# Performance work log

Measured on AMD Instinct MI355X. Metric: run time of the kernel, lower is better.

Reference implementation:

```python
import jax, jax.numpy as jnp
import numpy as np

LN_EPS = 1e-5

def setup_inputs() -> dict:
    key = jax.random.key(0)
    ks = jax.random.split(key, 5)
    B, S, Dv, Dl, V = 4, 576, 1024, 4096, 32000
    return {
        "vision_feats": jax.random.normal(ks[0], (B, S, Dv), dtype=jnp.float32),
        "W1_w": jax.random.normal(ks[1], (Dl, Dv), dtype=jnp.float32) * (Dv ** -0.5),
        "W1_b": jax.random.normal(ks[2], (Dl,), dtype=jnp.float32) * 0.02,
        "W2_w": jax.random.normal(ks[3], (V, Dl), dtype=jnp.float32) * (Dl ** -0.5),
        "llm_token_embed": jax.random.normal(ks[4], (V, Dl), dtype=jnp.float32) * 0.02,
    }

def reference(vision_feats, W1_w, W1_b, W2_w, llm_token_embed):
    # W1: (B,S,Dv) @ (Dv,Dl) + b -> (B,S,Dl)
    x = jnp.einsum('bsd,ed->bse', vision_feats, W1_w) + W1_b
    # layer_norm over last dim, no affine params
    mu = jnp.mean(x, axis=-1, keepdims=True)
    var = jnp.mean(jnp.square(x - mu), axis=-1, keepdims=True)
    xn = (x - mu) * jax.lax.rsqrt(var + LN_EPS)
    # W2 (no bias): (B,S,Dl) -> (B,S,V) vocab logits
    logits = jnp.einsum('bse,ve->bsv', xn, W2_w)
    P = jax.nn.softmax(logits, axis=-1)
    # softmax-weighted mixture of LLM token embeddings: (B,S,V) @ (V,Dl)
    F_align = jnp.einsum('bsv,ve->bse', P, llm_token_embed)
    return F_align
```

## Files before the change

kernel.cpp:

```cpp
#include <hip/hip_runtime.h>
#include <hip/hip_bf16.h>
#include <stdint.h>

typedef __bf16 bf16_t;
typedef __attribute__((ext_vector_type(8))) __bf16 bf16x8;
typedef __attribute__((ext_vector_type(4))) __bf16 bf16x4;
typedef __attribute__((ext_vector_type(4))) float f32x4;
typedef __attribute__((ext_vector_type(8))) unsigned short u16x8;

#define M_TOK 2304
#define DV    1024
#define DLAT  4096
#define VOCAB 32000

__device__ __forceinline__ float bf2f(unsigned short u) {
  union { unsigned int i; float f; } v; v.i = ((unsigned int)u) << 16; return v.f;
}
__device__ __forceinline__ bf16_t f2bf(float f) { return (bf16_t)f; }

#define GLOAD16(gp, lp) \
  __builtin_amdgcn_global_load_lds( \
      (const __attribute__((address_space(1))) unsigned int*)(const void*)(gp), \
      (__attribute__((address_space(3))) unsigned int*)(void*)(lp), 16, 0, 0)

constexpr int GBM = 128, GBN = 128, GBK = 32;

template<int EPI>
__global__ void __launch_bounds__(256, 3)
gemm_bb(const bf16_t* __restrict__ Ap, const bf16_t* __restrict__ Bp,
        void* __restrict__ Cp, const float* __restrict__ bias,
        int K, int ldc, int Mt)
{
  __shared__ __align__(16) bf16_t Al[3][GBM * GBK];
  __shared__ __align__(16) bf16_t Bl[3][GBN * GBK];

  const int nwg = gridDim.x;
  const int orig = blockIdx.x;
  const int q = nwg >> 3, r = nwg & 7;
  const int xcd = orig & 7, idx = orig >> 3;
  const int wg = (xcd < r ? xcd * (q + 1) : r * (q + 1) + (xcd - r) * q) + idx;
  const int mt = wg % Mt, nt = wg / Mt;
  const int m0 = mt * GBM, n0 = nt * GBN;

  const int t    = threadIdx.x;
  const int lane = t & 63, wv = t >> 6;
  const int wm = wv >> 1, wn = wv & 1;
  const int lr = lane & 15, kc = lane >> 4;

  f32x4 acc[4][4];
#pragma unroll
  for (int i = 0; i < 4; ++i)
#pragma unroll
    for (int j = 0; j < 4; ++j)
#pragma unroll
      for (int x = 0; x < 4; ++x) acc[i][j][x] = 0.0f;

  const int rql = lane >> 2;
  const int cbs = (((lane & 3) ^ ((lane >> 3) & 3)) * 16);
  const size_t rstride = (size_t)K * 2;

  const int sw8 = (kc ^ ((lr >> 1) & 3)) * 8;

  const int NT = K / GBK;

  auto STAGE = [&](int kt, int nb) {
    const size_t kb = (size_t)kt * GBK * 2;
    const char* ga = (const char*)Ap + (size_t)(m0 + wv * 32 + rql) * rstride + kb + cbs;
    char* la = (char*)&Al[nb][0] + wv * 2048;
    GLOAD16(ga, la);
    GLOAD16(ga + 16 * rstride, la + 1024);
    const char* gb = (const char*)Bp + (size_t)(n0 + wv * 32 + rql) * rstride + kb + cbs;
    char* lb = (char*)&Bl[nb][0] + wv * 2048;
    GLOAD16(gb, lb);
    GLOAD16(gb + 16 * rstride, lb + 1024);
  };

  auto COMPUTE = [&](int nb) {
    bf16x8 af[4], bfv[4];
#pragma unroll
    for (int f = 0; f < 4; ++f)
      af[f] = *(const bf16x8*)(&Al[nb][(wm * 64 + f * 16 + lr) * GBK + sw8]);
#pragma unroll
    for (int f = 0; f < 4; ++f)
      bfv[f] = *(const bf16x8*)(&Bl[nb][(wn * 64 + f * 16 + lr) * GBK + sw8]);
    __builtin_amdgcn_s_setprio(1);
#pragma unroll
    for (int i = 0; i < 4; ++i)
#pragma unroll
      for (int j = 0; j < 4; ++j)
        acc[i][j] = __builtin_amdgcn_mfma_f32_16x16x32_bf16(af[i], bfv[j], acc[i][j], 0, 0, 0);
    __builtin_amdgcn_s_setprio(0);
  };

  auto BARX = [&]() {
    asm volatile("s_waitcnt lgkmcnt(0)" ::: "memory");
    __builtin_amdgcn_s_barrier();
  };

  STAGE(0, 0);
  STAGE(1, 1);
  asm volatile("s_waitcnt vmcnt(4)" ::: "memory");
  __builtin_amdgcn_s_barrier();

  int bc = 0, bn = 1, bs = 2;
  for (int kt = 0; kt < NT - 2; ++kt) {
    STAGE(kt + 2, bs);
    COMPUTE(bc);
    asm volatile("s_waitcnt vmcnt(4)" ::: "memory");
    BARX();
    const int tmp = bc; bc = bn; bn = bs; bs = tmp;
  }
  COMPUTE(bc);
  asm volatile("s_waitcnt vmcnt(0)" ::: "memory");
  BARX();
  COMPUTE(bn);

#pragma unroll
  for (int j = 0; j < 4; ++j) {
    const int col = n0 + wn * 64 + j * 16 + lr;
    float bv = 0.0f;
    if (EPI == 0) bv = bias[col];
#pragma unroll
    for (int i = 0; i < 4; ++i) {
      const int row = m0 + wm * 64 + i * 16 + kc * 4;
      f32x4 a4 = acc[i][j];
      if (EPI == 1) {
        bf16_t* C = (bf16_t*)Cp;
#pragma unroll
        for (int x = 0; x < 4; ++x) C[(size_t)(row + x) * ldc + col] = f2bf(a4[x]);
      } else {
        float* C = (float*)Cp;
#pragma unroll
        for (int x = 0; x < 4; ++x) C[(size_t)(row + x) * ldc + col] = a4[x] + bv;
      }
    }
  }
}

constexpr int BM = 128, BN = 128, BK = 32;
constexpr int SA = 40;

__device__ __forceinline__ void bar_lds() {
  asm volatile("s_waitcnt lgkmcnt(0)" ::: "memory");
  __builtin_amdgcn_s_barrier();
}

template<int AMODE, int BMODE, int EPI>
__global__ void __launch_bounds__(256, 2)
gemm_k(const void* __restrict__ Ap, const float* __restrict__ Bp,
       void* __restrict__ Cp, const float* __restrict__ bias,
       int K, int lda, int ldb, int ldc, int Mt)
{
  __shared__ __align__(16) bf16_t Al[2][BM * SA];
  __shared__ __align__(16) bf16_t Bl[2][BN * SA];

  const int nwg = gridDim.x;
  const int orig = blockIdx.x;
  const int q = nwg >> 3, r = nwg & 7;
  const int xcd = orig & 7, idx = orig >> 3;
  const int wg = (xcd < r ? xcd * (q + 1) : r * (q + 1) + (xcd - r) * q) + idx;
  const int mt = wg % Mt, nt = wg / Mt;
  const int m0 = mt * BM, n0 = nt * BN;

  const int t    = threadIdx.x;
  const int lane = t & 63, wv = t >> 6;
  const int wm = wv >> 1, wn = wv & 1;
  const int lr = lane & 15, kc = lane >> 4;

  f32x4 acc[4][4];
#pragma unroll
  for (int i = 0; i < 4; ++i)
#pragma unroll
    for (int j = 0; j < 4; ++j)
#pragma unroll
      for (int x = 0; x < 4; ++x) acc[i][j][x] = 0.0f;

  const int sr = t >> 1, sh = t & 1;
  const int tv = t & 7, te = t >> 3;

  bf16x8 s1_ab0, s1_ab1;          bf16x8 s2_ab0, s2_ab1;
  f32x4  s1_af0, s1_af1, s1_af2, s1_af3;
  f32x4  s2_af0, s2_af1, s2_af2, s2_af3;
  f32x4  s1_b0, s1_b1, s1_b2, s1_b3;
  f32x4  s2_b0, s2_b1, s2_b2, s2_b3;

  const int NT = K / BK;

  auto LOADS1 = [&](int kt) {
    const int k0 = kt * BK;
    if (AMODE == 0) {
      const bf16_t* asrc = (const bf16_t*)Ap + (size_t)(m0 + sr) * lda + k0 + sh * 16;
      s1_ab0 = *(const bf16x8*)(asrc);
      s1_ab1 = *(const bf16x8*)(asrc + 8);
    } else {
      const float* asrc = (const float*)Ap + (size_t)(m0 + sr) * lda + k0 + sh * 16;
      s1_af0 = *(const f32x4*)(asrc);     s1_af1 = *(const f32x4*)(asrc + 4);
      s1_af2 = *(const f32x4*)(asrc + 8); s1_af3 = *(const f32x4*)(asrc + 12);
    }
    if (BMODE == 0) {
      const float* bsrc = Bp + (size_t)(n0 + sr) * ldb + k0 + sh * 16;
      s1_b0 = *(const f32x4*)(bsrc);     s1_b1 = *(const f32x4*)(bsrc + 4);
      s1_b2 = *(const f32x4*)(bsrc + 8); s1_b3 = *(const f32x4*)(bsrc + 12);
    } else {
      const float* bsrc = Bp + (size_t)(k0 + tv * 4) * ldb + n0 + te * 4;
      s1_b0 = *(const f32x4*)(bsrc);
      s1_b1 = *(const f32x4*)(bsrc + (size_t)ldb);
      s1_b2 = *(const f32x4*)(bsrc + (size_t)2 * ldb);
      s1_b3 = *(const f32x4*)(bsrc + (size_t)3 * ldb);
    }
  };
  auto LOADS2 = [&](int kt) {
    const int k0 = kt * BK;
    if (AMODE == 0) {
      const bf16_t* asrc = (const bf16_t*)Ap + (size_t)(m0 + sr) * lda + k0 + sh * 16;
      s2_ab0 = *(const bf16x8*)(asrc);
      s2_ab1 = *(const bf16x8*)(asrc + 8);
    } else {
      const float* asrc = (const float*)Ap + (size_t)(m0 + sr) * lda + k0 + sh * 16;
      s2_af0 = *(const f32x4*)(asrc);     s2_af1 = *(const f32x4*)(asrc + 4);
      s2_af2 = *(const f32x4*)(asrc + 8); s2_af3 = *(const f32x4*)(asrc + 12);
    }
    if (BMODE == 0) {
      const float* bsrc = Bp + (size_t)(n0 + sr) * ldb + k0 + sh * 16;
      s2_b0 = *(const f32x4*)(bsrc);     s2_b1 = *(const f32x4*)(bsrc + 4);
      s2_b2 = *(const f32x4*)(bsrc + 8); s2_b3 = *(const f32x4*)(bsrc + 12);
    } else {
      const float* bsrc = Bp + (size_t)(k0 + tv * 4) * ldb + n0 + te * 4;
      s2_b0 = *(const f32x4*)(bsrc);
      s2_b1 = *(const f32x4*)(bsrc + (size_t)ldb);
      s2_b2 = *(const f32x4*)(bsrc + (size_t)2 * ldb);
      s2_b3 = *(const f32x4*)(bsrc + (size_t)3 * ldb);
    }
  };

  auto STORE1 = [&](int nb) {
    {
      bf16x8 w0, w1;
      if (AMODE == 0) { w0 = s1_ab0; w1 = s1_ab1; }
      else {
#pragma unroll
        for (int c = 0; c < 4; ++c) {
          w0[c] = f2bf(s1_af0[c]); w0[c + 4] = f2bf(s1_af1[c]);
          w1[c] = f2bf(s1_af2[c]); w1[c + 4] = f2bf(s1_af3[c]);
        }
      }
      bf16_t* dst = &Al[nb][sr * SA + sh * 16];
      *(bf16x8*)(dst) = w0; *(bf16x8*)(dst + 8) = w1;
    }
    if (BMODE == 0) {
      bf16x8 w0, w1;
#pragma unroll
      for (int c = 0; c < 4; ++c) {
        w0[c] = f2bf(s1_b0[c]); w0[c + 4] = f2bf(s1_b1[c]);
        w1[c] = f2bf(s1_b2[c]); w1[c + 4] = f2bf(s1_b3[c]);
      }
      bf16_t* dst = &Bl[nb][sr * SA + sh * 16];
      *(bf16x8*)(dst) = w0; *(bf16x8*)(dst + 8) = w1;
    } else {
#pragma unroll
      for (int i = 0; i < 4; ++i) {
        bf16x4 w4;
        w4[0] = f2bf(s1_b0[i]); w4[1] = f2bf(s1_b1[i]);
        w4[2] = f2bf(s1_b2[i]); w4[3] = f2bf(s1_b3[i]);
        *(bf16x4*)(&Bl[nb][(te * 4 + i) * SA + tv * 4]) = w4;
      }
    }
  };
  auto STORE2 = [&](int nb) {
    {
      bf16x8 w0, w1;
      if (AMODE == 0) { w0 = s2_ab0; w1 = s2_ab1; }
      else {
#pragma unroll
        for (int c = 0; c < 4; ++c) {
          w0[c] = f2bf(s2_af0[c]); w0[c + 4] = f2bf(s2_af1[c]);
          w1[c] = f2bf(s2_af2[c]); w1[c + 4] = f2bf(s2_af3[c]);
        }
      }
      bf16_t* dst = &Al[nb][sr * SA + sh * 16];
      *(bf16x8*)(dst) = w0; *(bf16x8*)(dst + 8) = w1;
    }
    if (BMODE == 0) {
      bf16x8 w0, w1;
#pragma unroll
      for (int c = 0; c < 4; ++c) {
        w0[c] = f2bf(s2_b0[c]); w0[c + 4] = f2bf(s2_b1[c]);
        w1[c] = f2bf(s2_b2[c]); w1[c + 4] = f2bf(s2_b3[c]);
      }
      bf16_t* dst = &Bl[nb][sr * SA + sh * 16];
      *(bf16x8*)(dst) = w0; *(bf16x8*)(dst + 8) = w1;
    } else {
#pragma unroll
      for (int i = 0; i < 4; ++i) {
        bf16x4 w4;
        w4[0] = f2bf(s2_b0[i]); w4[1] = f2bf(s2_b1[i]);
        w4[2] = f2bf(s2_b2[i]); w4[3] = f2bf(s2_b3[i]);
        *(bf16x4*)(&Bl[nb][(te * 4 + i) * SA + tv * 4]) = w4;
      }
    }
  };

  auto COMPUTE = [&](int nb) {
    bf16x8 af[4], bfv[4];
#pragma unroll
    for (int f = 0; f < 4; ++f)
      af[f] = *(const bf16x8*)(&Al[nb][(wm * 64 + f * 16 + lr) * SA + kc * 8]);
#pragma unroll
    for (int f = 0; f < 4; ++f)
      bfv[f] = *(const bf16x8*)(&Bl[nb][(wn * 64 + f * 16 + lr) * SA + kc * 8]);
    __builtin_amdgcn_s_setprio(1);
#pragma unroll
    for (int i = 0; i < 4; ++i)
#pragma unroll
      for (int j = 0; j < 4; ++j)
        acc[i][j] = __builtin_amdgcn_mfma_f32_16x16x32_bf16(af[i], bfv[j], acc[i][j], 0, 0, 0);
    __builtin_amdgcn_s_setprio(0);
  };

  LOADS1(0);
  LOADS2(1);
  STORE1(0);
  bar_lds();

  const int NIT = NT / 2 - 1;
  for (int it = 0; it < NIT; ++it) {
    LOADS1(2 * it + 2);
    COMPUTE(0);
    STORE2(1);
    bar_lds();
    LOADS2(2 * it + 3);
    COMPUTE(1);
    STORE1(0);
    bar_lds();
  }
  COMPUTE(0);
  STORE2(1);
  bar_lds();
  COMPUTE(1);

#pragma unroll
  for (int j = 0; j < 4; ++j) {
    const int col = n0 + wn * 64 + j * 16 + lr;
    float bv = 0.0f;
    if (EPI == 0) bv = bias[col];
#pragma unroll
    for (int i = 0; i < 4; ++i) {
      const int row = m0 + wm * 64 + i * 16 + kc * 4;
      f32x4 a4 = acc[i][j];
      if (EPI == 0) {
        float* C = (float*)Cp;
#pragma unroll
        for (int x = 0; x < 4; ++x) C[(size_t)(row + x) * ldc + col] = a4[x] + bv;
      } else if (EPI == 1) {
        bf16_t* C = (bf16_t*)Cp;
#pragma unroll
        for (int x = 0; x < 4; ++x) C[(size_t)(row + x) * ldc + col] = f2bf(a4[x]);
      } else {
        float* C = (float*)Cp;
#pragma unroll
        for (int x = 0; x < 4; ++x) C[(size_t)(row + x) * ldc + col] = a4[x];
      }
    }
  }
}

__global__ void __launch_bounds__(256)
cvt_bf16_k(const float* __restrict__ in, bf16_t* __restrict__ out, long n8)
{
  const long stride = (long)gridDim.x * 256;
  for (long i = (long)blockIdx.x * 256 + threadIdx.x; i < n8; i += stride) {
    f32x4 a = *(const f32x4*)(in + i * 8);
    f32x4 b = *(const f32x4*)(in + i * 8 + 4);
    bf16x8 o;
#pragma unroll
    for (int j = 0; j < 4; ++j) { o[j] = f2bf(a[j]); o[j + 4] = f2bf(b[j]); }
    *(bf16x8*)(out + i * 8) = o;
  }
}

__global__ void __launch_bounds__(256)
embT_k(const float* __restrict__ E, bf16_t* __restrict__ ET)
{
  __shared__ bf16_t tl[64][72];
  const int vb = blockIdx.x % (VOCAB / 64);
  const int eb = blockIdx.x / (VOCAB / 64);
  const int v0 = vb * 64, e0 = eb * 64;
  const int t = threadIdx.x;

  const int rr = t >> 4, c4 = (t & 15) * 4;
#pragma unroll
  for (int p = 0; p < 4; ++p) {
    const float* src = E + (size_t)(v0 + rr + p * 16) * DLAT + e0 + c4;
    f32x4 a = *(const f32x4*)src;
#pragma unroll
    for (int j = 0; j < 4; ++j) tl[c4 + j][rr + p * 16] = f2bf(a[j]);
  }
  __syncthreads();

  const int el = t >> 3, v8 = (t & 7) * 8;
#pragma unroll
  for (int p = 0; p < 2; ++p) {
    bf16x8 o = *(const bf16x8*)(&tl[el + p * 32][v8]);
    *(bf16x8*)(ET + (size_t)(e0 + el + p * 32) * VOCAB + v0 + v8) = o;
  }
}

__global__ void __launch_bounds__(256)
ln_k(const float* __restrict__ x, bf16_t* __restrict__ xn)
{
  __shared__ float sm[4];
  const int row = blockIdx.x, t = threadIdx.x;
  const float* xr = x + (size_t)row * DLAT;
  f32x4 v[4];
#pragma unroll
  for (int i = 0; i < 4; ++i) v[i] = *(const f32x4*)(xr + (t + i * 256) * 4);

  float s = 0.0f;
#pragma unroll
  for (int i = 0; i < 4; ++i)
#pragma unroll
    for (int j = 0; j < 4; ++j) s += v[i][j];
#pragma unroll
  for (int o = 32; o > 0; o >>= 1) s += __shfl_xor(s, o, 64);
  if ((t & 63) == 0) sm[t >> 6] = s;
  __syncthreads();
  const float mean = (sm[0] + sm[1] + sm[2] + sm[3]) * (1.0f / DLAT);
  __syncthreads();

  float qv = 0.0f;
#pragma unroll
  for (int i = 0; i < 4; ++i)
#pragma unroll
    for (int j = 0; j < 4; ++j) { float d = v[i][j] - mean; qv += d * d; }
#pragma unroll
  for (int o = 32; o > 0; o >>= 1) qv += __shfl_xor(qv, o, 64);
  if ((t & 63) == 0) sm[t >> 6] = qv;
  __syncthreads();
  const float varr = (sm[0] + sm[1] + sm[2] + sm[3]) * (1.0f / DLAT);
  const float rs = rsqrtf(varr + 1e-5f);

  bf16_t* outr = xn + (size_t)row * DLAT;
#pragma unroll
  for (int i = 0; i < 4; ++i) {
    bf16x4 o;
#pragma unroll
    for (int j = 0; j < 4; ++j) o[j] = f2bf((v[i][j] - mean) * rs);
    *(bf16x4*)(outr + (t + i * 256) * 4) = o;
  }
}

__global__ void __launch_bounds__(256)
softmax_k(bf16_t* __restrict__ L)
{
  __shared__ __align__(16) bf16_t rs_[VOCAB];
  __shared__ float sm[4];
  const int row = blockIdx.x, t = threadIdx.x;
  bf16_t* lrow = L + (size_t)row * VOCAB;
  const int NF = VOCAB / 8;

  float m = -3.0e38f;
  for (int f = t; f < NF; f += 256) {
    u16x8 u = *(const u16x8*)(&lrow[f * 8]);
    *(u16x8*)(&rs_[f * 8]) = u;
#pragma unroll
    for (int j = 0; j < 8; ++j) m = fmaxf(m, bf2f(u[j]));
  }
#pragma unroll
  for (int o = 32; o > 0; o >>= 1) m = fmaxf(m, __shfl_xor(m, o, 64));
  if ((t & 63) == 0) sm[t >> 6] = m;
  __syncthreads();
  m = fmaxf(fmaxf(sm[0], sm[1]), fmaxf(sm[2], sm[3]));
  __syncthreads();

  float s = 0.0f;
  for (int f = t; f < NF; f += 256) {
    u16x8 u = *(const u16x8*)(&rs_[f * 8]);
#pragma unroll
    for (int j = 0; j < 8; ++j) s += __expf(bf2f(u[j]) - m);
  }
#pragma unroll
  for (int o = 32; o > 0; o >>= 1) s += __shfl_xor(s, o, 64);
  if ((t & 63) == 0) sm[t >> 6] = s;
  __syncthreads();
  const float inv = 1.0f / (sm[0] + sm[1] + sm[2] + sm[3]);

  for (int f = t; f < NF; f += 256) {
    u16x8 u = *(const u16x8*)(&rs_[f * 8]);
    bf16x8 o;
#pragma unroll
    for (int j = 0; j < 8; ++j) o[j] = f2bf(__expf(bf2f(u[j]) - m) * inv);
    *(bf16x8*)(&lrow[f * 8]) = o;
  }
}

extern "C" void kernel_launch(void* const* d_in, const int* in_sizes, int n_in,
                              void* d_out, int out_size, void* d_ws, size_t ws_size,
                              hipStream_t stream)
{
  (void)in_sizes; (void)n_in; (void)out_size;
  const float* vision = (const float*)d_in[0];
  const float* W1w    = (const float*)d_in[1];
  const float* W1b    = (const float*)d_in[2];
  const float* W2w    = (const float*)d_in[3];
  const float* Emb    = (const float*)d_in[4];
  float* out = (float*)d_out;

  char* ws = (char*)d_ws;
  bf16_t* xn     = (bf16_t*)ws;
  bf16_t* logits = (bf16_t*)(ws + 18874368);
  float*  xbuf   = (float*)(ws + 166330368);
  bf16_t* wslot  = (bf16_t*)(ws + 204079104);
  bf16_t* xnv    = (bf16_t*)(ws + 466223104);
  bf16_t* w1b    = (bf16_t*)(ws + 470941696);
  const size_t NEED = 479330304ull;

  const int Mt = M_TOK / GBM;

  if (ws_size >= NEED) {
    cvt_bf16_k<<<dim3(512), dim3(256), 0, stream>>>(vision, xnv, (long)M_TOK * DV / 8);
    cvt_bf16_k<<<dim3(512), dim3(256), 0, stream>>>(W1w, w1b, (long)DLAT * DV / 8);
    gemm_bb<0><<<dim3(Mt * (DLAT / GBN)), dim3(256), 0, stream>>>(
        xnv, w1b, xbuf, W1b, DV, DLAT, Mt);
    ln_k<<<dim3(M_TOK), dim3(256), 0, stream>>>(xbuf, xn);
    cvt_bf16_k<<<dim3(2048), dim3(256), 0, stream>>>(W2w, wslot, (long)VOCAB * DLAT / 8);
    gemm_bb<1><<<dim3(Mt * (VOCAB / GBN)), dim3(256), 0, stream>>>(
        xn, wslot, logits, nullptr, DLAT, VOCAB, Mt);
    embT_k<<<dim3((VOCAB / 64) * (DLAT / 64)), dim3(256), 0, stream>>>(Emb, wslot);
    softmax_k<<<dim3(M_TOK), dim3(256), 0, stream>>>(logits);
    gemm_bb<2><<<dim3(Mt * (DLAT / GBN)), dim3(256), 0, stream>>>(
        logits, wslot, out, nullptr, VOCAB, DLAT, Mt);
  } else {
    gemm_k<1, 0, 0><<<dim3((M_TOK / BM) * (DLAT / BN)), dim3(256), 0, stream>>>(
        vision, W1w, xbuf, W1b, DV, DV, DV, DLAT, M_TOK / BM);
    ln_k<<<dim3(M_TOK), dim3(256), 0, stream>>>(xbuf, xn);
    gemm_k<0, 0, 1><<<dim3((M_TOK / BM) * (VOCAB / BN)), dim3(256), 0, stream>>>(
        xn, W2w, logits, nullptr, DLAT, DLAT, DLAT, VOCAB, M_TOK / BM);
    softmax_k<<<dim3(M_TOK), dim3(256), 0, stream>>>(logits);
    gemm_k<0, 1, 2><<<dim3((M_TOK / BM) * (DLAT / BN)), dim3(256), 0, stream>>>(
        logits, Emb, out, nullptr, VOCAB, VOCAB, DLAT, DLAT, M_TOK / BM);
  }
}
```

Before: 1.955 ms.

## Use 256-row 512-thread GEMM tiles for vocab GEMMs with split-K final GEMM

Adds a gemm256 kernel with 256xBN tiles, 8 waves, a triple-buffered direct-to-LDS pipeline and staged loads interleaved with MFMA phases. It replaces the 128x128 kernel for the logits GEMM and for the softmax-times-embedding GEMM. The latter is split into two K halves whose partials are summed by a small add kernel. It also removes the fp32 fallback path that ran when the workspace was too small. The intent is more data reuse per tile and better CU fill on the final GEMM, at the cost of extra partial-sum traffic and an extra launch.

Result: slower. 2.300 ms (+17.7%).

```diff
diff --git a/kernel.cpp b/kernel.cpp
--- a/kernel.cpp
+++ b/kernel.cpp
@@ -22,6 +22,148 @@
   __builtin_amdgcn_global_load_lds( \
       (const __attribute__((address_space(1))) unsigned int*)(const void*)(gp), \
       (__attribute__((address_space(3))) unsigned int*)(void*)(lp), 16, 0, 0)
+
+template<int BN_, int WM_, int WN_, int EPI, int MINW>
+__global__ void __launch_bounds__(512, MINW)
+gemm256(const bf16_t* __restrict__ Ap, const bf16_t* __restrict__ Bp,
+        void* __restrict__ Cp0, void* __restrict__ Cp1,
+        int Ksplit, int ld, int ldc, int Mt, int Nt)
+{
+  constexpr int WMR = 256 / WM_;
+  constexpr int NFM = WMR / 16;
+  constexpr int NFN = (BN_ / WN_) / 16;
+  constexpr int PM  = NFM / 4;
+  constexpr int BLOADS = BN_ / 128;
+  constexpr int L = 2 + BLOADS;
+
+  __shared__ __align__(16) bf16_t Al[3][256 * 32];
+  __shared__ __align__(16) bf16_t Bl[3][BN_ * 32];
+
+  const int nwg = gridDim.x;
+  const int orig = blockIdx.x;
+  const int q = nwg >> 3, r = nwg & 7;
+  const int xcd = orig & 7, idx = orig >> 3;
+  const int wg = (xcd < r ? xcd * (q + 1) : r * (q + 1) + (xcd - r) * q) + idx;
+  const int mt = wg % Mt;
+  const int nt = (wg / Mt) % Nt;
+  const int sp = wg / (Mt * Nt);
+  const int m0 = mt * 256, n0 = nt * BN_;
+  const int kb0 = sp * Ksplit;
+
+  const int t    = threadIdx.x;
+  const int lane = t & 63, wv = t >> 6;
+  const int wm = wv / WN_, wn = wv % WN_;
+  const int lr = lane & 15, kc = lane >> 4;
+
+  const int rql = lane >> 2;
+  const int cbs = (((lane & 3) ^ ((lane >> 3) & 3)) * 16);
+  const int sw8 = (kc ^ ((lr >> 1) & 3)) * 8;
+  const size_t rstride = (size_t)ld * 2;
+
+  f32x4 acc[NFM][NFN];
+#pragma unroll
+  for (int i = 0; i < NFM; ++i)
+#pragma unroll
+    for (int j = 0; j < NFN; ++j)
+#pragma unroll
+      for (int x = 0; x < 4; ++x) acc[i][j][x] = 0.0f;
+
+  const int NT = Ksplit / 32;
+
+  auto SG = [&](int kt, int nb, int which) {
+    const size_t kb = (size_t)(kb0 + kt * 32) * 2;
+    if (which < 2) {
+      const char* g = (const char*)Ap + (size_t)(m0 + wv * 32 + rql) * rstride
+                      + (size_t)which * 16 * rstride + kb + cbs;
+      char* l = (char*)&Al[nb][0] + wv * 2048 + which * 1024;
+      GLOAD16(g, l);
+    } else if (BLOADS == 2) {
+      const int w2 = which - 2;
+      const char* g = (const char*)Bp + (size_t)(n0 + wv * 32 + rql) * rstride
+                      + (size_t)w2 * 16 * rstride + kb + cbs;
+      char* l = (char*)&Bl[nb][0] + wv * 2048 + w2 * 1024;
+      GLOAD16(g, l);
+    } else {
+      const char* g = (const char*)Bp + (size_t)(n0 + wv * 16 + rql) * rstride + kb + cbs;
+      char* l = (char*)&Bl[nb][0] + wv * 1024;
+      GLOAD16(g, l);
+    }
+  };
+
+  auto TILE = [&](int bc, int bs, int kt, int stg, int wait) {
+    bf16x8 bfv[NFN];
+#pragma unroll
+    for (int p = 0; p < 4; ++p) {
+      bf16x8 af[PM];
+      if (p == 0) {
+#pragma unroll
+        for (int g = 0; g < NFN; ++g)
+          bfv[g] = *(const bf16x8*)(&Bl[bc][(wn * 64 + g * 16 + lr) * 32 + sw8]);
+      }
+#pragma unroll
+      for (int s = 0; s < PM; ++s)
+        af[s] = *(const bf16x8*)(&Al[bc][(wm * WMR + (p * PM + s) * 16 + lr) * 32 + sw8]);
+      if (stg) {
+        if (p < 2) SG(kt + 2, bs, p);
+        else if (p - 2 < BLOADS) SG(kt + 2, bs, p);
+      }
+      if (p == 3) {
+        if (wait == 1) {
+          if constexpr (L == 4) asm volatile("s_waitcnt vmcnt(4)" ::: "memory");
+          else                  asm volatile("s_waitcnt vmcnt(3)" ::: "memory");
+        } else if (wait == 2) {
+          asm volatile("s_waitcnt vmcnt(0)" ::: "memory");
+        }
+      }
+      __builtin_amdgcn_s_barrier();
+      __builtin_amdgcn_s_setprio(1);
+#pragma unroll
+      for (int s = 0; s < PM; ++s)
+#pragma unroll
+        for (int g = 0; g < NFN; ++g)
+          acc[p * PM + s][g] =
+            __builtin_amdgcn_mfma_f32_16x16x32_bf16(af[s], bfv[g], acc[p * PM + s][g], 0, 0, 0);
+      __builtin_amdgcn_s_setprio(0);
+    }
+  };
+
+#pragma unroll
+  for (int w = 0; w < L; ++w) SG(0, 0, w);
+#pragma unroll
+  for (int w = 0; w < L; ++w) SG(1, 1, w);
+  if constexpr (L == 4) asm volatile("s_waitcnt vmcnt(4)" ::: "memory");
+  else                  asm volatile("s_waitcnt vmcnt(3)" ::: "memory");
+  __builtin_amdgcn_s_barrier();
+
+  int c0 = 0, c1 = 1, c2 = 2;
+  int kt = 0;
+  for (; kt < NT - 2; ++kt) {
+    TILE(c0, c2, kt, 1, 1);
+    const int tmp = c0; c0 = c1; c1 = c2; c2 = tmp;
+  }
+  TILE(c0, c2, kt, 0, 2);
+  { const int tmp = c0; c0 = c1; c1 = c2; c2 = tmp; }
+  TILE(c0, c2, kt + 1, 0, 0);
+
+  float* Cf = (EPI == 2) ? (sp == 0 ? (float*)Cp0 : (float*)Cp1) : (float*)Cp0;
+#pragma unroll
+  for (int j = 0; j < NFN; ++j) {
+    const int col = n0 + wn * 64 + j * 16 + lr;
+#pragma unroll
+    for (int i = 0; i < NFM; ++i) {
+      const int row = m0 + wm * WMR + i * 16 + kc * 4;
+      f32x4 a4 = acc[i][j];
+      if (EPI == 1) {
+        bf16_t* C = (bf16_t*)Cp0;
+#pragma unroll
+        for (int x = 0; x < 4; ++x) C[(size_t)(row + x) * ldc + col] = f2bf(a4[x]);
+      } else {
+#pragma unroll
+        for (int x = 0; x < 4; ++x) Cf[(size_t)(row + x) * ldc + col] = a4[x];
+      }
+    }
+  }
+}
 
 constexpr int GBM = 128, GBN = 128, GBK = 32;
 
@@ -57,9 +199,8 @@
 
   const int rql = lane >> 2;
   const int cbs = (((lane & 3) ^ ((lane >> 3) & 3)) * 16);
+  const int sw8 = (kc ^ ((lr >> 1) & 3)) * 8;
   const size_t rstride = (size_t)K * 2;
-
-  const int sw8 = (kc ^ ((lr >> 1) & 3)) * 8;
 
   const int NT = K / GBK;
 
@@ -137,230 +278,16 @@
   }
 }
 
-constexpr int BM = 128, BN = 128, BK = 32;
-constexpr int SA = 40;
-
-__device__ __forceinline__ void bar_lds() {
-  asm volatile("s_waitcnt lgkmcnt(0)" ::: "memory");
-  __builtin_amdgcn_s_barrier();
-}
-
-template<int AMODE, int BMODE, int EPI>
-__global__ void __launch_bounds__(256, 2)
-gemm_k(const void* __restrict__ Ap, const float* __restrict__ Bp,
-       void* __restrict__ Cp, const float* __restrict__ bias,
-       int K, int lda, int ldb, int ldc, int Mt)
-{
-  __shared__ __align__(16) bf16_t Al[2][BM * SA];
-  __shared__ __align__(16) bf16_t Bl[2][BN * SA];
-
-  const int nwg = gridDim.x;
-  const int orig = blockIdx.x;
-  const int q = nwg >> 3, r = nwg & 7;
-  const int xcd = orig & 7, idx = orig >> 3;
-  const int wg = (xcd < r ? xcd * (q + 1) : r * (q + 1) + (xcd - r) * q) + idx;
-  const int mt = wg % Mt, nt = wg / Mt;
-  const int m0 = mt * BM, n0 = nt * BN;
-
-  const int t    = threadIdx.x;
-  const int lane = t & 63, wv = t >> 6;
-  const int wm = wv >> 1, wn = wv & 1;
-  const int lr = lane & 15, kc = lane >> 4;
-
-  f32x4 acc[4][4];
-#pragma unroll
-  for (int i = 0; i < 4; ++i)
-#pragma unroll
-    for (int j = 0; j < 4; ++j)
-#pragma unroll
-      for (int x = 0; x < 4; ++x) acc[i][j][x] = 0.0f;
-
-  const int sr = t >> 1, sh = t & 1;
-  const int tv = t & 7, te = t >> 3;
-
-  bf16x8 s1_ab0, s1_ab1;          bf16x8 s2_ab0, s2_ab1;
-  f32x4  s1_af0, s1_af1, s1_af2, s1_af3;
-  f32x4  s2_af0, s2_af1, s2_af2, s2_af3;
-  f32x4  s1_b0, s1_b1, s1_b2, s1_b3;
-  f32x4  s2_b0, s2_b1, s2_b2, s2_b3;
-
-  const int NT = K / BK;
-
-  auto LOADS1 = [&](int kt) {
-    const int k0 = kt * BK;
-    if (AMODE == 0) {
-      const bf16_t* asrc = (const bf16_t*)Ap + (size_t)(m0 + sr) * lda + k0 + sh * 16;
-      s1_ab0 = *(const bf16x8*)(asrc);
-      s1_ab1 = *(const bf16x8*)(asrc + 8);
-    } else {
-      const float* asrc = (const float*)Ap + (size_t)(m0 + sr) * lda + k0 + sh * 16;
-      s1_af0 = *(const f32x4*)(asrc);     s1_af1 = *(const f32x4*)(asrc + 4);
-      s1_af2 = *(const f32x4*)(asrc + 8); s1_af3 = *(const f32x4*)(asrc + 12);
-    }
-    if (BMODE == 0) {
-      const float* bsrc = Bp + (size_t)(n0 + sr) * ldb + k0 + sh * 16;
-      s1_b0 = *(const f32x4*)(bsrc);     s1_b1 = *(const f32x4*)(bsrc + 4);
-      s1_b2 = *(const f32x4*)(bsrc + 8); s1_b3 = *(const f32x4*)(bsrc + 12);
-    } else {
-      const float* bsrc = Bp + (size_t)(k0 + tv * 4) * ldb + n0 + te * 4;
-      s1_b0 = *(const f32x4*)(bsrc);
-      s1_b1 = *(const f32x4*)(bsrc + (size_t)ldb);
-      s1_b2 = *(const f32x4*)(bsrc + (size_t)2 * ldb);
-      s1_b3 = *(const f32x4*)(bsrc + (size_t)3 * ldb);
-    }
-  };
-  auto LOADS2 = [&](int kt) {
-    const int k0 = kt * BK;
-    if (AMODE == 0) {
-      const bf16_t* asrc = (const bf16_t*)Ap + (size_t)(m0 + sr) * lda + k0 + sh * 16;
-      s2_ab0 = *(const bf16x8*)(asrc);
-      s2_ab1 = *(const bf16x8*)(asrc + 8);
-    } else {
-      const float* asrc = (const float*)Ap + (size_t)(m0 + sr) * lda + k0 + sh * 16;
-      s2_af0 = *(const f32x4*)(asrc);     s2_af1 = *(const f32x4*)(asrc + 4);
-      s2_af2 = *(const f32x4*)(asrc + 8); s2_af3 = *(const f32x4*)(asrc + 12);
-    }
-    if (BMODE == 0) {
-      const float* bsrc = Bp + (size_t)(n0 + sr) * ldb + k0 + sh * 16;
-      s2_b0 = *(const f32x4*)(bsrc);     s2_b1 = *(const f32x4*)(bsrc + 4);
-      s2_b2 = *(const f32x4*)(bsrc + 8); s2_b3 = *(const f32x4*)(bsrc + 12);
-    } else {
-      const float* bsrc = Bp + (size_t)(k0 + tv * 4) * ldb + n0 + te * 4;
-      s2_b0 = *(const f32x4*)(bsrc);
-      s2_b1 = *(const f32x4*)(bsrc + (size_t)ldb);
-      s2_b2 = *(const f32x4*)(bsrc + (size_t)2 * ldb);
-      s2_b3 = *(const f32x4*)(bsrc + (size_t)3 * ldb);
-    }
-  };
-
-  auto STORE1 = [&](int nb) {
-    {
-      bf16x8 w0, w1;
-      if (AMODE == 0) { w0 = s1_ab0; w1 = s1_ab1; }
-      else {
-#pragma unroll
-        for (int c = 0; c < 4; ++c) {
-          w0[c] = f2bf(s1_af0[c]); w0[c + 4] = f2bf(s1_af1[c]);
-          w1[c] = f2bf(s1_af2[c]); w1[c + 4] = f2bf(s1_af3[c]);
-        }
-      }
-      bf16_t* dst = &Al[nb][sr * SA + sh * 16];
-      *(bf16x8*)(dst) = w0; *(bf16x8*)(dst + 8) = w1;
-    }
-    if (BMODE == 0) {
-      bf16x8 w0, w1;
-#pragma unroll
-      for (int c = 0; c < 4; ++c) {
-        w0[c] = f2bf(s1_b0[c]); w0[c + 4] = f2bf(s1_b1[c]);
-        w1[c] = f2bf(s1_b2[c]); w1[c + 4] = f2bf(s1_b3[c]);
-      }
-      bf16_t* dst = &Bl[nb][sr * SA + sh * 16];
-      *(bf16x8*)(dst) = w0; *(bf16x8*)(dst + 8) = w1;
-    } else {
-#pragma unroll
-      for (int i = 0; i < 4; ++i) {
-        bf16x4 w4;
-        w4[0] = f2bf(s1_b0[i]); w4[1] = f2bf(s1_b1[i]);
-        w4[2] = f2bf(s1_b2[i]); w4[3] = f2bf(s1_b3[i]);
-        *(bf16x4*)(&Bl[nb][(te * 4 + i) * SA + tv * 4]) = w4;
-      }
-    }
-  };
-  auto STORE2 = [&](int nb) {
-    {
-      bf16x8 w0, w1;
-      if (AMODE == 0) { w0 = s2_ab0; w1 = s2_ab1; }
-      else {
-#pragma unroll
-        for (int c = 0; c < 4; ++c) {
-          w0[c] = f2bf(s2_af0[c]); w0[c + 4] = f2bf(s2_af1[c]);
-          w1[c] = f2bf(s2_af2[c]); w1[c + 4] = f2bf(s2_af3[c]);
-        }
-      }
-      bf16_t* dst = &Al[nb][sr * SA + sh * 16];
-      *(bf16x8*)(dst) = w0; *(bf16x8*)(dst + 8) = w1;
-    }
-    if (BMODE == 0) {
-      bf16x8 w0, w1;
-#pragma unroll
-      for (int c = 0; c < 4; ++c) {
-        w0[c] = f2bf(s2_b0[c]); w0[c + 4] = f2bf(s2_b1[c]);
-        w1[c] = f2bf(s2_b2[c]); w1[c + 4] = f2bf(s2_b3[c]);
-      }
-      bf16_t* dst = &Bl[nb][sr * SA + sh * 16];
-      *(bf16x8*)(dst) = w0; *(bf16x8*)(dst + 8) = w1;
-    } else {
-#pragma unroll
-      for (int i = 0; i < 4; ++i) {
-        bf16x4 w4;
-        w4[0] = f2bf(s2_b0[i]); w4[1] = f2bf(s2_b1[i]);
-        w4[2] = f2bf(s2_b2[i]); w4[3] = f2bf(s2_b3[i]);
-        *(bf16x4*)(&Bl[nb][(te * 4 + i) * SA + tv * 4]) = w4;
-      }
-    }
-  };
-
-  auto COMPUTE = [&](int nb) {
-    bf16x8 af[4], bfv[4];
-#pragma unroll
-    for (int f = 0; f < 4; ++f)
-      af[f] = *(const bf16x8*)(&Al[nb][(wm * 64 + f * 16 + lr) * SA + kc * 8]);
-#pragma unroll
-    for (int f = 0; f < 4; ++f)
-      bfv[f] = *(const bf16x8*)(&Bl[nb][(wn * 64 + f * 16 + lr) * SA + kc * 8]);
-    __builtin_amdgcn_s_setprio(1);
-#pragma unroll
-    for (int i = 0; i < 4; ++i)
-#pragma unroll
-      for (int j = 0; j < 4; ++j)
-        acc[i][j] = __builtin_amdgcn_mfma_f32_16x16x32_bf16(af[i], bfv[j], acc[i][j], 0, 0, 0);
-    __builtin_amdgcn_s_setprio(0);
-  };
-
-  LOADS1(0);
-  LOADS2(1);
-  STORE1(0);
-  bar_lds();
-
-  const int NIT = NT / 2 - 1;
-  for (int it = 0; it < NIT; ++it) {
-    LOADS1(2 * it + 2);
-    COMPUTE(0);
-    STORE2(1);
-    bar_lds();
-    LOADS2(2 * it + 3);
-    COMPUTE(1);
-    STORE1(0);
-    bar_lds();
-  }
-  COMPUTE(0);
-  STORE2(1);
-  bar_lds();
-  COMPUTE(1);
-
-#pragma unroll
-  for (int j = 0; j < 4; ++j) {
-    const int col = n0 + wn * 64 + j * 16 + lr;
-    float bv = 0.0f;
-    if (EPI == 0) bv = bias[col];
-#pragma unroll
-    for (int i = 0; i < 4; ++i) {
-      const int row = m0 + wm * 64 + i * 16 + kc * 4;
-      f32x4 a4 = acc[i][j];
-      if (EPI == 0) {
-        float* C = (float*)Cp;
-#pragma unroll
-        for (int x = 0; x < 4; ++x) C[(size_t)(row + x) * ldc + col] = a4[x] + bv;
-      } else if (EPI == 1) {
-        bf16_t* C = (bf16_t*)Cp;
-#pragma unroll
-        for (int x = 0; x < 4; ++x) C[(size_t)(row + x) * ldc + col] = f2bf(a4[x]);
-      } else {
-        float* C = (float*)Cp;
-#pragma unroll
-        for (int x = 0; x < 4; ++x) C[(size_t)(row + x) * ldc + col] = a4[x];
-      }
-    }
+__global__ void __launch_bounds__(256)
+addk(float* __restrict__ out, const float* __restrict__ part, int n4)
+{
+  const int stride = gridDim.x * 256;
+  for (int i = blockIdx.x * 256 + threadIdx.x; i < n4; i += stride) {
+    f32x4 a = *(const f32x4*)(out + i * 4);
+    f32x4 b = *(const f32x4*)(part + i * 4);
+#pragma unroll
+    for (int x = 0; x < 4; ++x) a[x] += b[x];
+    *(f32x4*)(out + i * 4) = a;
   }
 }
 
@@ -497,7 +424,7 @@
                               void* d_out, int out_size, void* d_ws, size_t ws_size,
                               hipStream_t stream)
 {
-  (void)in_sizes; (void)n_in; (void)out_size;
+  (void)in_sizes; (void)n_in; (void)out_size; (void)ws_size;
   const float* vision = (const float*)d_in[0];
   const float* W1w    = (const float*)d_in[1];
   const float* W1b    = (const float*)d_in[2];
@@ -512,31 +439,26 @@
   bf16_t* wslot  = (bf16_t*)(ws + 204079104);
   bf16_t* xnv    = (bf16_t*)(ws + 466223104);
   bf16_t* w1b    = (bf16_t*)(ws + 470941696);
-  const size_t NEED = 479330304ull;
-
-  const int Mt = M_TOK / GBM;
-
-  if (ws_size >= NEED) {
-    cvt_bf16_k<<<dim3(512), dim3(256), 0, stream>>>(vision, xnv, (long)M_TOK * DV / 8);
-    cvt_bf16_k<<<dim3(512), dim3(256), 0, stream>>>(W1w, w1b, (long)DLAT * DV / 8);
-    gemm_bb<0><<<dim3(Mt * (DLAT / GBN)), dim3(256), 0, stream>>>(
-        xnv, w1b, xbuf, W1b, DV, DLAT, Mt);
-    ln_k<<<dim3(M_TOK), dim3(256), 0, stream>>>(xbuf, xn);
-    cvt_bf16_k<<<dim3(2048), dim3(256), 0, stream>>>(W2w, wslot, (long)VOCAB * DLAT / 8);
-    gemm_bb<1><<<dim3(Mt * (VOCAB / GBN)), dim3(256), 0, stream>>>(
-        xn, wslot, logits, nullptr, DLAT, VOCAB, Mt);
-    embT_k<<<dim3((VOCAB / 64) * (DLAT / 64)), dim3(256), 0, stream>>>(Emb, wslot);
-    softmax_k<<<dim3(M_TOK), dim3(256), 0, stream>>>(logits);
-    gemm_bb<2><<<dim3(Mt * (DLAT / GBN)), dim3(256), 0, stream>>>(
-        logits, wslot, out, nullptr, VOCAB, DLAT, Mt);
-  } else {
-    gemm_k<1, 0, 0><<<dim3((M_TOK / BM) * (DLAT / BN)), dim3(256), 0, stream>>>(
-        vision, W1w, xbuf, W1b, DV, DV, DV, DLAT, M_TOK / BM);
-    ln_k<<<dim3(M_TOK), dim3(256), 0, stream>>>(xbuf, xn);
-    gemm_k<0, 0, 1><<<dim3((M_TOK / BM) * (VOCAB / BN)), dim3(256), 0, stream>>>(
-        xn, W2w, logits, nullptr, DLAT, DLAT, DLAT, VOCAB, M_TOK / BM);
-    softmax_k<<<dim3(M_TOK), dim3(256), 0, stream>>>(logits);
-    gemm_k<0, 1, 2><<<dim3((M_TOK / BM) * (DLAT / BN)), dim3(256), 0, stream>>>(
-        logits, Emb, out, nullptr, VOCAB, VOCAB, DLAT, DLAT, M_TOK / BM);
-  }
-}
+
+  cvt_bf16_k<<<dim3(512), dim3(256), 0, stream>>>(vision, xnv, (long)M_TOK * DV / 8);
+  cvt_bf16_k<<<dim3(512), dim3(256), 0, stream>>>(W1w, w1b, (long)DLAT * DV / 8);
+
+  gemm_bb<0><<<dim3((M_TOK / GBM) * (DLAT / GBN)), dim3(256), 0, stream>>>(
+      xnv, w1b, xbuf, W1b, DV, DLAT, M_TOK / GBM);
+
+  ln_k<<<dim3(M_TOK), dim3(256), 0, stream>>>(xbuf, xn);
+
+  cvt_bf16_k<<<dim3(2048), dim3(256), 0, stream>>>(W2w, wslot, (long)VOCAB * DLAT / 8);
+
+  gemm256<256, 2, 4, 1, 2><<<dim3(9 * 125), dim3(512), 0, stream>>>(
+      xn, wslot, logits, nullptr, DLAT, DLAT, VOCAB, 9, 125);
+
+  embT_k<<<dim3((VOCAB / 64) * (DLAT / 64)), dim3(256), 0, stream>>>(Emb, wslot);
+
+  softmax_k<<<dim3(M_TOK), dim3(256), 0, stream>>>(logits);
+
+  gemm256<128, 4, 2, 2, 4><<<dim3(9 * 32 * 2), dim3(512), 0, stream>>>(
+      logits, wslot, out, xbuf, VOCAB / 2, VOCAB, DLAT, 9, 32);
+
+  addk<<<dim3(1024), dim3(256), 0, stream>>>(out, xbuf, (M_TOK * DLAT) / 4);
+}
```
